# Kernel optimization log

Measured on AMD Instinct MI355X. Metric: run time of the kernel, lower is better.

Reference implementation:

```python
import jax, jax.numpy as jnp
import numpy as np

DIM = 1024
NUM_HEADS = 16
HEAD_DIM = DIM // NUM_HEADS


def _rope_tables(seq_len, dim, dtype):
    # matches llama_rotary_embedding: inv_freq over even indices of head_dim
    inv_freq = 1.0 / (10000.0 ** (jnp.arange(0, dim, 2, dtype=jnp.float32) / dim))
    t = jnp.arange(seq_len, dtype=jnp.float32)
    freqs = jnp.outer(t, inv_freq)  # [S, dim/2]
    return jnp.cos(freqs).astype(dtype), jnp.sin(freqs).astype(dtype)


def _apply_rope(x, cos_emb, sin_emb):
    # x: [B, H, S, hd]; takes interleaved halves, concatenates rotated halves
    x1 = x[..., 0::2]
    x2 = x[..., 1::2]
    return jnp.concatenate((x1 * cos_emb - x2 * sin_emb,
                            x1 * sin_emb + x2 * cos_emb), axis=-1)


def setup_inputs() -> dict:
    key = jax.random.key(0)
    k_x, k_qkv, k_out, k_b = jax.random.split(key, 4)
    B, S, D = 2, 2048, DIM
    x = jax.random.normal(k_x, (B, S, D), dtype=jnp.float32)
    # torch nn.Linear weights are [out_features, in_features]
    w_qkv = jax.random.normal(k_qkv, (3 * D, D), dtype=jnp.float32) * (1.0 / np.sqrt(D))
    w_out = jax.random.normal(k_out, (D, D), dtype=jnp.float32) * (1.0 / np.sqrt(D))
    b_out = jax.random.normal(k_b, (D,), dtype=jnp.float32) * 0.01
    return {"x": x, "w_qkv": w_qkv, "w_out": w_out, "b_out": b_out}


def reference(x, w_qkv, w_out, b_out):
    B, S, D = x.shape
    H, hd = NUM_HEADS, HEAD_DIM
    qkv = jnp.einsum('bsd,ed->bse', x, w_qkv)  # [B, S, 3D]
    q, k, v = jnp.split(qkv, 3, axis=-1)
    # [B, S, D] -> [B, H, S, hd]
    q, k, v = (t.reshape(B, S, H, hd).transpose(0, 2, 1, 3) for t in (q, k, v))
    cos_emb, sin_emb = _rope_tables(S, hd, x.dtype)  # [S, hd/2]
    q = _apply_rope(q, cos_emb, sin_emb)
    k = _apply_rope(k, cos_emb, sin_emb)
    scores = jnp.einsum('bhqd,bhkd->bhqk', q, k) / jnp.sqrt(jnp.asarray(hd, x.dtype))
    attn = jax.nn.softmax(scores, axis=-1)
    out = jnp.einsum('bhqk,bhkd->bhqd', attn, v)
    out = out.transpose(0, 2, 1, 3).reshape(B, S, D)
    return jnp.einsum('bsd,ed->bse', out, w_out) + b_out
```

## Files before the change

kernel.cpp:

```cpp
#include <hip/hip_runtime.h>
#include <math.h>

typedef __bf16 bf16_t;
typedef bf16_t bf16x8 __attribute__((ext_vector_type(8)));
typedef bf16_t bf16x4 __attribute__((ext_vector_type(4)));
typedef short  s16x4  __attribute__((ext_vector_type(4)));
typedef float  f32x4  __attribute__((ext_vector_type(4)));

#define DIM_   1024
#define NHEADS 16
#define HDIM   64
#define SEQ    2048
#define BATCH  2

#define QK_SCALE 0.18033688011112042f

__device__ __forceinline__ s16x4 as_s16x4(bf16x4 v) {
    union { bf16x4 b; s16x4 s; } u; u.b = v; return u.s;
}

__device__ __forceinline__ void gld16(const bf16_t* g, bf16_t* l) {
    __builtin_amdgcn_global_load_lds(
        (const __attribute__((address_space(1))) void*)g,
        (__attribute__((address_space(3))) void*)l, 16, 0, 0);
}

#define XCNT   (4096u * 1024u)
#define WQCNT  (3072u * 1024u)
#define WOCNT  (1024u * 1024u)
__global__ __launch_bounds__(256) void cast3(const float* __restrict__ s0,
                                             const float* __restrict__ s1,
                                             const float* __restrict__ s2,
                                             bf16_t* __restrict__ d0,
                                             bf16_t* __restrict__ d1,
                                             bf16_t* __restrict__ d2) {
    size_t i = ((size_t)blockIdx.x * 256 + threadIdx.x) * 8;
    const float* s; bf16_t* d; size_t off;
    if (i < XCNT)               { s = s0; d = d0; off = i; }
    else if (i < XCNT + WQCNT)  { s = s1; d = d1; off = i - XCNT; }
    else                        { s = s2; d = d2; off = i - XCNT - WQCNT; }
    float4 a = *(const float4*)(s + off);
    float4 b = *(const float4*)(s + off + 4);
    bf16x8 o = { (bf16_t)a.x, (bf16_t)a.y, (bf16_t)a.z, (bf16_t)a.w,
                 (bf16_t)b.x, (bf16_t)b.y, (bf16_t)b.z, (bf16_t)b.w };
    *(bf16x8*)(d + off) = o;
}

template <bool QKV>
__global__ __launch_bounds__(256) void gemm_lds(const bf16_t* __restrict__ A,
                                                const bf16_t* __restrict__ B,
                                                const float* __restrict__ bias,
                                                void* __restrict__ Cout,
                                                bf16_t* __restrict__ vt,
                                                int M, int N, int K) {
    __shared__ __align__(16) bf16_t As[2][128 * 32];
    __shared__ __align__(16) bf16_t Bs[2][128 * 32];
    const int tid  = threadIdx.x;
    const int m0   = blockIdx.y * 128;
    const int n0   = blockIdx.x * 128;
    const int w    = tid >> 6;
    const int lane = tid & 63;
    const int m16  = lane & 15;
    const int quad = lane >> 4;
    const int wm   = (w >> 1) * 64;
    const int wn   = (w & 1) * 64;
    const int lrow = lane >> 2;
    const int lcol = (lane & 3) * 8;

    const bf16_t* pa0 = A + (size_t)(m0 + w * 16 + lrow) * K + lcol;
    const bf16_t* pb0 = B + (size_t)(n0 + w * 16 + lrow) * K + lcol;
    const int sOffA0 = (w * 16) * 32;
    const int sOffA1 = (64 + w * 16) * 32;

    gld16(pa0, (bf16_t*)As + sOffA0);
    gld16(pa0 + (size_t)64 * K, (bf16_t*)As + sOffA1);
    gld16(pb0, (bf16_t*)Bs + sOffA0);
    gld16(pb0 + (size_t)64 * K, (bf16_t*)Bs + sOffA1);
    __syncthreads();

    f32x4 acc[4][4] = {};
    int buf = 0;

    for (int k0 = 0; k0 < K; k0 += 32) {
        const int nb = buf ^ 1;
        if (k0 + 32 < K) {
            gld16(pa0 + k0 + 32, (bf16_t*)As + nb * 4096 + sOffA0);
            gld16(pa0 + (size_t)64 * K + k0 + 32, (bf16_t*)As + nb * 4096 + sOffA1);
            gld16(pb0 + k0 + 32, (bf16_t*)Bs + nb * 4096 + sOffA0);
            gld16(pb0 + (size_t)64 * K + k0 + 32, (bf16_t*)Bs + nb * 4096 + sOffA1);
        }
        const bf16_t* sA = (const bf16_t*)As + buf * 4096;
        const bf16_t* sB = (const bf16_t*)Bs + buf * 4096;
        bf16x8 af[4], bfr[4];
#pragma unroll
        for (int i = 0; i < 4; ++i)
            af[i] = *(const bf16x8*)(sA + (wm + i * 16 + m16) * 32 + quad * 8);
#pragma unroll
        for (int j = 0; j < 4; ++j)
            bfr[j] = *(const bf16x8*)(sB + (wn + j * 16 + m16) * 32 + quad * 8);
#pragma unroll
        for (int i = 0; i < 4; ++i)
#pragma unroll
            for (int j = 0; j < 4; ++j)
                acc[i][j] = __builtin_amdgcn_mfma_f32_16x16x32_bf16(af[i], bfr[j], acc[i][j], 0, 0, 0);
        __syncthreads();
        buf = nb;
    }

    if (QKV && n0 >= 2 * DIM_) {
        const int b      = m0 >> 11;
        const int s_base = (m0 & (SEQ - 1)) + wm;
#pragma unroll
        for (int j = 0; j < 4; ++j) {
            const int cit = wn + j * 16 + m16;
            const int h   = ((n0 - 2 * DIM_) >> 6) + (cit >> 6);
            const int d   = cit & 63;
            bf16_t* vrow = vt + ((size_t)(b * 16 + h) * 64 + d) * SEQ + s_base;
#pragma unroll
            for (int i = 0; i < 4; ++i) {
                bf16x4 ov = { (bf16_t)acc[i][j][0], (bf16_t)acc[i][j][1],
                              (bf16_t)acc[i][j][2], (bf16_t)acc[i][j][3] };
                *(bf16x4*)(vrow + i * 16 + quad * 4) = ov;
            }
        }
    } else if (QKV) {
        bf16_t* C = (bf16_t*)Cout;
#pragma unroll
        for (int i = 0; i < 4; ++i)
#pragma unroll
            for (int j = 0; j < 4; ++j) {
                const int col = n0 + wn + j * 16 + m16;
#pragma unroll
                for (int r = 0; r < 4; ++r)
                    C[(size_t)(m0 + wm + i * 16 + quad * 4 + r) * N + col] = (bf16_t)acc[i][j][r];
            }
    } else {
        float* C = (float*)Cout;
#pragma unroll
        for (int j = 0; j < 4; ++j) {
            const int col = n0 + wn + j * 16 + m16;
            const float bv = bias[col];
#pragma unroll
            for (int i = 0; i < 4; ++i)
#pragma unroll
                for (int r = 0; r < 4; ++r)
                    C[(size_t)(m0 + wm + i * 16 + quad * 4 + r) * N + col] = acc[i][j][r] + bv;
        }
    }
}

__global__ __launch_bounds__(256) void gemm_out64(const bf16_t* __restrict__ A,
                                                  const bf16_t* __restrict__ B,
                                                  const float* __restrict__ bias,
                                                  float* __restrict__ C,
                                                  int M, int N, int K) {
    __shared__ __align__(16) bf16_t As[2][128 * 32];
    __shared__ __align__(16) bf16_t Bs[2][64 * 32];
    const int tid  = threadIdx.x;
    const int m0   = blockIdx.y * 128;
    const int n0   = blockIdx.x * 64;
    const int w    = tid >> 6;
    const int lane = tid & 63;
    const int m16  = lane & 15;
    const int quad = lane >> 4;
    const int wm   = (w >> 1) * 64;
    const int wn   = (w & 1) * 32;
    const int lrow = lane >> 2;
    const int lcol = (lane & 3) * 8;

    const bf16_t* pa0 = A + (size_t)(m0 + w * 16 + lrow) * K + lcol;
    const bf16_t* pb0 = B + (size_t)(n0 + w * 16 + lrow) * K + lcol;
    const int sOff0 = (w * 16) * 32;
    const int sOff1 = (64 + w * 16) * 32;

    gld16(pa0, (bf16_t*)As + sOff0);
    gld16(pa0 + (size_t)64 * K, (bf16_t*)As + sOff1);
    gld16(pb0, (bf16_t*)Bs + sOff0);
    __syncthreads();

    f32x4 acc[4][2] = {};
    int buf = 0;

    for (int k0 = 0; k0 < K; k0 += 32) {
        const int nb = buf ^ 1;
        if (k0 + 32 < K) {
            gld16(pa0 + k0 + 32, (bf16_t*)As + nb * 4096 + sOff0);
            gld16(pa0 + (size_t)64 * K + k0 + 32, (bf16_t*)As + nb * 4096 + sOff1);
            gld16(pb0 + k0 + 32, (bf16_t*)Bs + nb * 2048 + sOff0);
        }
        const bf16_t* sA = (const bf16_t*)As + buf * 4096;
        const bf16_t* sB = (const bf16_t*)Bs + buf * 2048;
        bf16x8 af[4], bfr[2];
#pragma unroll
        for (int i = 0; i < 4; ++i)
            af[i] = *(const bf16x8*)(sA + (wm + i * 16 + m16) * 32 + quad * 8);
#pragma unroll
        for (int j = 0; j < 2; ++j)
            bfr[j] = *(const bf16x8*)(sB + (wn + j * 16 + m16) * 32 + quad * 8);
#pragma unroll
        for (int i = 0; i < 4; ++i)
#pragma unroll
            for (int j = 0; j < 2; ++j)
                acc[i][j] = __builtin_amdgcn_mfma_f32_16x16x32_bf16(af[i], bfr[j], acc[i][j], 0, 0, 0);
        __syncthreads();
        buf = nb;
    }

#pragma unroll
    for (int j = 0; j < 2; ++j) {
        const int col = n0 + wn + j * 16 + m16;
        const float bv = bias[col];
#pragma unroll
        for (int i = 0; i < 4; ++i)
#pragma unroll
            for (int r = 0; r < 4; ++r)
                C[(size_t)(m0 + wm + i * 16 + quad * 4 + r) * N + col] = acc[i][j][r] + bv;
    }
}

__global__ __launch_bounds__(256) void rope_bf16(bf16_t* __restrict__ qkv) {
    __shared__ float ctab[8][32];
    __shared__ float stab[8][32];
    const int tid = threadIdx.x;
    const int sl  = tid >> 5, j = tid & 31;
    const int s   = (int)((blockIdx.x * 8 + sl) & (SEQ - 1));
    const float freq = exp2f(-0.41524101186092029f * (float)j);
    float sn, cs;
    sincosf((float)s * freq, &sn, &cs);
    ctab[sl][j] = cs;
    stab[sl][j] = sn;
    __syncthreads();

    const int gid   = blockIdx.x * 256 + tid;
    const int m     = gid >> 5;
    const int rr    = gid & 31;
    const int which = rr >> 4;
    const int hh    = rr & 15;
    const float osc = (which == 0) ? QK_SCALE : 1.0f;

    bf16_t* p = qkv + (size_t)m * (3 * DIM_) + which * DIM_ + hh * HDIM;
    union { bf16_t e[64]; bf16x8 v[8]; } X, O;
#pragma unroll
    for (int i = 0; i < 8; ++i) X.v[i] = *(const bf16x8*)(p + i * 8);
#pragma unroll
    for (int t = 0; t < 32; ++t) {
        const float x1 = (float)X.e[2 * t];
        const float x2 = (float)X.e[2 * t + 1];
        const float c  = ctab[sl][t];
        const float s2 = stab[sl][t];
        O.e[t]      = (bf16_t)((x1 * c - x2 * s2) * osc);
        O.e[32 + t] = (bf16_t)((x1 * s2 + x2 * c) * osc);
    }
#pragma unroll
    for (int i = 0; i < 8; ++i) *(bf16x8*)(p + i * 8) = O.v[i];
}

__global__ __launch_bounds__(256) void attn_mfma(const bf16_t* __restrict__ qkv,
                                                 const bf16_t* __restrict__ vt,
                                                 bf16_t* __restrict__ out) {
    __shared__ __align__(16) char smem[37888];
    bf16_t* Ks0  = (bf16_t*)smem;
    bf16_t* Vt0  = (bf16_t*)(smem + 9216);
    bf16_t* Ks1  = (bf16_t*)(smem + 18432);
    bf16_t* Vt1  = (bf16_t*)(smem + 27648);
    float*  Ored = (float*)smem;
    float*  Lred = (float*)(smem + 36864);

    const int tid  = threadIdx.x;
    const int w    = tid >> 6;
    const int lane = tid & 63;
    const int m16  = lane & 15;
    const int quad = lane >> 4;
    const int bh   = blockIdx.y;
    const int b    = bh >> 4;
    const int hh   = bh & 15;
    const int q0   = blockIdx.x * 64;

    const size_t rs = 3 * DIM_;
    const bf16_t* qbase = qkv + (size_t)(b * SEQ) * rs + hh * HDIM;
    const bf16_t* kbase = qbase + DIM_;
    const bf16_t* vtg   = vt + (size_t)bh * 64 * SEQ;

    bf16x8 qf[4][2];
#pragma unroll
    for (int n = 0; n < 4; ++n)
#pragma unroll
        for (int kt = 0; kt < 2; ++kt)
            qf[n][kt] = *(const bf16x8*)(qbase + (size_t)(q0 + n * 16 + m16) * rs + kt * 32 + quad * 8);

    f32x4 o[4][4] = {};
    float lp[4] = {};

    const int srow = tid >> 3;
    const int sc8  = (tid & 7) * 8;

    bf16x8 kreg[2], vreg[2];

#pragma unroll
    for (int p = 0; p < 2; ++p) {
        const int row = srow + p * 32;
        kreg[p] = *(const bf16x8*)(kbase + (size_t)row * rs + sc8);
        vreg[p] = *(const bf16x8*)(vtg + (size_t)row * SEQ + sc8);
    }
#pragma unroll
    for (int p = 0; p < 2; ++p) {
        const int row = srow + p * 32;
        *(bf16x8*)(&Ks0[row * 72 + sc8]) = kreg[p];
        *(bf16x8*)(&Vt0[row * 72 + sc8]) = vreg[p];
    }
    __syncthreads();

    const bf16_t* kg0 = kbase + (size_t)(64 + srow) * rs + sc8;
    const bf16_t* kg1 = kg0 + (size_t)32 * rs;
    const bf16_t* vg0 = vtg + (size_t)srow * SEQ + 64 + sc8;
    const bf16_t* vg1 = vg0 + (size_t)32 * SEQ;
    const size_t kadv = (size_t)64 * rs;

#define ATTN_BODY(T, KS, VS, KSN, VSN)                                             \
    do {                                                                           \
        const int tt = (T);                                                        \
        if (tt < 31) {                                                             \
            kreg[0] = *(const bf16x8*)(kg0);                                       \
            kreg[1] = *(const bf16x8*)(kg1);                                       \
            vreg[0] = *(const bf16x8*)(vg0);                                       \
            vreg[1] = *(const bf16x8*)(vg1);                                       \
            kg0 += kadv; kg1 += kadv; vg0 += 64; vg1 += 64;                        \
        }                                                                          \
        bf16x8 ak0 = *(const bf16x8*)(&KS[(w * 16 + m16) * 72 + 0 * 32 + quad * 8]); \
        bf16x8 ak1 = *(const bf16x8*)(&KS[(w * 16 + m16) * 72 + 1 * 32 + quad * 8]); \
        bf16x4 va[4];                                                              \
        _Pragma("unroll")                                                          \
        for (int ds = 0; ds < 4; ++ds)                                             \
            va[ds] = *(const bf16x4*)(&VS[(ds * 16 + m16) * 72 + w * 16 + quad * 4]); \
        s16x4 pb[4];                                                               \
        _Pragma("unroll")                                                          \
        for (int n = 0; n < 4; ++n) {                                              \
            f32x4 c = {};                                                          \
            c = __builtin_amdgcn_mfma_f32_16x16x32_bf16(ak0, qf[n][0], c, 0, 0, 0); \
            c = __builtin_amdgcn_mfma_f32_16x16x32_bf16(ak1, qf[n][1], c, 0, 0, 0); \
            bf16x4 pv;                                                             \
            _Pragma("unroll")                                                      \
            for (int r = 0; r < 4; ++r) {                                          \
                const float pp = __builtin_amdgcn_exp2f(c[r]);                     \
                lp[n] += pp;                                                       \
                pv[r] = (bf16_t)pp;                                                \
            }                                                                      \
            pb[n] = as_s16x4(pv);                                                  \
        }                                                                          \
        __builtin_amdgcn_s_setprio(1);                                             \
        _Pragma("unroll")                                                          \
        for (int ds = 0; ds < 4; ++ds)                                             \
            _Pragma("unroll")                                                      \
            for (int n = 0; n < 4; ++n)                                            \
                o[ds][n] = __builtin_amdgcn_mfma_f32_16x16x16bf16_1k(               \
                    as_s16x4(va[ds]), pb[n], o[ds][n], 0, 0, 0);                   \
        __builtin_amdgcn_s_setprio(0);                                             \
        if (tt < 31) {                                                             \
            _Pragma("unroll")                                                      \
            for (int p = 0; p < 2; ++p) {                                          \
                const int row = srow + p * 32;                                     \
                *(bf16x8*)(&KSN[row * 72 + sc8]) = kreg[p];                        \
                *(bf16x8*)(&VSN[row * 72 + sc8]) = vreg[p];                        \
            }                                                                      \
        }                                                                          \
        __syncthreads();                                                           \
    } while (0)

    for (int t = 0; t < 32; t += 2) {
        ATTN_BODY(t,     Ks0, Vt0, Ks1, Vt1);
        ATTN_BODY(t + 1, Ks1, Vt1, Ks0, Vt0);
    }
#undef ATTN_BODY

#pragma unroll
    for (int n = 0; n < 4; ++n) {
        lp[n] += __shfl_xor(lp[n], 16);
        lp[n] += __shfl_xor(lp[n], 32);
    }
    if (quad == 0) {
#pragma unroll
        for (int n = 0; n < 4; ++n) Lred[w * 64 + n * 16 + m16] = lp[n];
    }
    __syncthreads();
    const float linv = 1.0f / (Lred[lane] + Lred[64 + lane] + Lred[128 + lane] + Lred[192 + lane]);

    const size_t obase = (size_t)(b * SEQ + q0 + lane) * DIM_ + hh * HDIM;
#pragma unroll
    for (int p = 0; p < 4; ++p) {
        __syncthreads();
#pragma unroll
        for (int n = 0; n < 4; ++n)
#pragma unroll
            for (int r = 0; r < 4; ++r)
                Ored[w * 1040 + (quad * 4 + r) * 65 + n * 16 + m16] = o[p][n][r];
        __syncthreads();
        union { bf16_t e[4]; bf16x4 v; } ob;
#pragma unroll
        for (int d = 0; d < 4; ++d) {
            const int dd = w * 4 + d;
            const float v = Ored[dd * 65 + lane] + Ored[1040 + dd * 65 + lane] +
                            Ored[2080 + dd * 65 + lane] + Ored[3120 + dd * 65 + lane];
            ob.e[d] = (bf16_t)(v * linv);
        }
        *(bf16x4*)(out + obase + p * 16 + w * 4) = ob.v;
    }
}

extern "C" void kernel_launch(void* const* d_in, const int* in_sizes, int n_in,
                              void* d_out, int out_size, void* d_ws, size_t ws_size,
                              hipStream_t stream) {
    const float* x     = (const float*)d_in[0];
    const float* w_qkv = (const float*)d_in[1];
    const float* w_out = (const float*)d_in[2];
    const float* b_out = (const float*)d_in[3];
    float* out = (float*)d_out;

    const int M = BATCH * SEQ;

    bf16_t* qkv_b  = (bf16_t*)d_ws;
    bf16_t* attn_b = qkv_b + (size_t)M * 3 * DIM_;
    bf16_t* vt_b   = attn_b + (size_t)M * DIM_;
    bf16_t* xb     = vt_b + (size_t)BATCH * NHEADS * HDIM * SEQ;
    bf16_t* wqkvb  = xb + (size_t)M * DIM_;
    bf16_t* woutb  = wqkvb + (size_t)3 * DIM_ * DIM_;

    cast3<<<(XCNT + WQCNT + WOCNT) / (256 * 8), 256, 0, stream>>>(
        x, w_qkv, w_out, xb, wqkvb, woutb);

    gemm_lds<true><<<dim3(3 * DIM_ / 128, M / 128), 256, 0, stream>>>(
        xb, wqkvb, nullptr, qkv_b, vt_b, M, 3 * DIM_, DIM_);

    rope_bf16<<<(M * 2 * NHEADS) / 256, 256, 0, stream>>>(qkv_b);

    attn_mfma<<<dim3(SEQ / 64, BATCH * NHEADS), 256, 0, stream>>>(qkv_b, vt_b, attn_b);

    gemm_out64<<<dim3(DIM_ / 64, M / 128), 256, 0, stream>>>(
        attn_b, woutb, b_out, out, M, DIM_, DIM_);
}
```

Baseline: 206.8 us.

## Software-pipeline attention loop: overlap PV MFMAs of previous tile with QK of current

Restructures the attention inner loop so each iteration computes QK scores and exp for the current K/V tile while issuing the PV MFMAs for the previous tile's probabilities and V fragments. A prologue handles tile 0 and an epilogue drains the last PV. The aim is to break the dependency between exp conversion and the PV MFMAs so the matrix units stay busy. In exchange it keeps two sets of P and V fragments in registers, which raises register pressure and could lower occupancy.

```diff
diff --git a/kernel.cpp b/kernel.cpp
--- a/kernel.cpp
+++ b/kernel.cpp
@@ -316,7 +316,45 @@
     const bf16_t* vg1 = vg0 + (size_t)32 * SEQ;
     const size_t kadv = (size_t)64 * rs;
 
-#define ATTN_BODY(T, KS, VS, KSN, VSN)                                             \
+    s16x4  pbA[4], pbB[4];
+    bf16x4 vaA[4], vaB[4];
+
+    {
+        kreg[0] = *(const bf16x8*)(kg0);
+        kreg[1] = *(const bf16x8*)(kg1);
+        vreg[0] = *(const bf16x8*)(vg0);
+        vreg[1] = *(const bf16x8*)(vg1);
+        kg0 += kadv; kg1 += kadv; vg0 += 64; vg1 += 64;
+
+        bf16x8 ak0 = *(const bf16x8*)(&Ks0[(w * 16 + m16) * 72 + 0 * 32 + quad * 8]);
+        bf16x8 ak1 = *(const bf16x8*)(&Ks0[(w * 16 + m16) * 72 + 1 * 32 + quad * 8]);
+#pragma unroll
+        for (int ds = 0; ds < 4; ++ds)
+            vaA[ds] = *(const bf16x4*)(&Vt0[(ds * 16 + m16) * 72 + w * 16 + quad * 4]);
+#pragma unroll
+        for (int n = 0; n < 4; ++n) {
+            f32x4 c = {};
+            c = __builtin_amdgcn_mfma_f32_16x16x32_bf16(ak0, qf[n][0], c, 0, 0, 0);
+            c = __builtin_amdgcn_mfma_f32_16x16x32_bf16(ak1, qf[n][1], c, 0, 0, 0);
+            bf16x4 pv;
+#pragma unroll
+            for (int r = 0; r < 4; ++r) {
+                const float pp = __builtin_amdgcn_exp2f(c[r]);
+                lp[n] += pp;
+                pv[r] = (bf16_t)pp;
+            }
+            pbA[n] = as_s16x4(pv);
+        }
+#pragma unroll
+        for (int p = 0; p < 2; ++p) {
+            const int row = srow + p * 32;
+            *(bf16x8*)(&Ks1[row * 72 + sc8]) = kreg[p];
+            *(bf16x8*)(&Vt1[row * 72 + sc8]) = vreg[p];
+        }
+        __syncthreads();
+    }
+
+#define ATTN_BODY(T, KS, VS, KSN, VSN, PBc, VAc, PBp, VAp)                         \
     do {                                                                           \
         const int tt = (T);                                                        \
         if (tt < 31) {                                                             \
@@ -328,11 +366,9 @@
         }                                                                          \
         bf16x8 ak0 = *(const bf16x8*)(&KS[(w * 16 + m16) * 72 + 0 * 32 + quad * 8]); \
         bf16x8 ak1 = *(const bf16x8*)(&KS[(w * 16 + m16) * 72 + 1 * 32 + quad * 8]); \
-        bf16x4 va[4];                                                              \
         _Pragma("unroll")                                                          \
         for (int ds = 0; ds < 4; ++ds)                                             \
-            va[ds] = *(const bf16x4*)(&VS[(ds * 16 + m16) * 72 + w * 16 + quad * 4]); \
-        s16x4 pb[4];                                                               \
+            VAc[ds] = *(const bf16x4*)(&VS[(ds * 16 + m16) * 72 + w * 16 + quad * 4]); \
         _Pragma("unroll")                                                          \
         for (int n = 0; n < 4; ++n) {                                              \
             f32x4 c = {};                                                          \
@@ -345,7 +381,7 @@
                 lp[n] += pp;                                                       \
                 pv[r] = (bf16_t)pp;                                                \
             }                                                                      \
-            pb[n] = as_s16x4(pv);                                                  \
+            PBc[n] = as_s16x4(pv);                                                 \
         }                                                                          \
         __builtin_amdgcn_s_setprio(1);                                             \
         _Pragma("unroll")                                                          \
@@ -353,7 +389,7 @@
             _Pragma("unroll")                                                      \
             for (int n = 0; n < 4; ++n)                                            \
                 o[ds][n] = __builtin_amdgcn_mfma_f32_16x16x16bf16_1k(               \
-                    as_s16x4(va[ds]), pb[n], o[ds][n], 0, 0, 0);                   \
+                    as_s16x4(VAp[ds]), PBp[n], o[ds][n], 0, 0, 0);                 \
         __builtin_amdgcn_s_setprio(0);                                             \
         if (tt < 31) {                                                             \
             _Pragma("unroll")                                                      \
@@ -366,11 +402,21 @@
         __syncthreads();                                                           \
     } while (0)
 
-    for (int t = 0; t < 32; t += 2) {
-        ATTN_BODY(t,     Ks0, Vt0, Ks1, Vt1);
-        ATTN_BODY(t + 1, Ks1, Vt1, Ks0, Vt0);
-    }
+    for (int t = 1; t < 31; t += 2) {
+        ATTN_BODY(t,     Ks1, Vt1, Ks0, Vt0, pbB, vaB, pbA, vaA);
+        ATTN_BODY(t + 1, Ks0, Vt0, Ks1, Vt1, pbA, vaA, pbB, vaB);
+    }
+    ATTN_BODY(31, Ks1, Vt1, Ks0, Vt0, pbB, vaB, pbA, vaA);
 #undef ATTN_BODY
+
+    __builtin_amdgcn_s_setprio(1);
+#pragma unroll
+    for (int ds = 0; ds < 4; ++ds)
+#pragma unroll
+        for (int n = 0; n < 4; ++n)
+            o[ds][n] = __builtin_amdgcn_mfma_f32_16x16x16bf16_1k(
+                as_s16x4(vaB[ds]), pbB[n], o[ds][n], 0, 0, 0);
+    __builtin_amdgcn_s_setprio(0);
 
 #pragma unroll
     for (int n = 0; n < 4; ++n) {
```

Measured after the change: 204.5 us. Within noise of the previous version (-1.1%).

## Store K per-head contiguous and V in MFMA tile order, drop attention LDS staging

Applied to the files above, without the earlier changes.

The QKV GEMM epilogue now writes Q, K (head-major, contiguous per sequence row) and V (pre-tiled into 16-key blocks matching the MFMA operand layout) into separate buffers. The attention kernel then loads K and V fragments straight from global memory into registers with a two-tile register double-buffer, removing the LDS staging and per-tile __syncthreads. This cuts shared memory use and barriers and may raise occupancy, but every wave now reads K/V from global/L2 independently instead of sharing an LDS copy. The K epilogue also uses scattered scalar stores.

```diff
diff --git a/kernel.cpp b/kernel.cpp
--- a/kernel.cpp
+++ b/kernel.cpp
@@ -46,11 +46,10 @@
     *(bf16x8*)(d + off) = o;
 }
 
-template <bool QKV>
-__global__ __launch_bounds__(256) void gemm_lds(const bf16_t* __restrict__ A,
+__global__ __launch_bounds__(256) void gemm_qkv(const bf16_t* __restrict__ A,
                                                 const bf16_t* __restrict__ B,
-                                                const float* __restrict__ bias,
-                                                void* __restrict__ Cout,
+                                                bf16_t* __restrict__ qb,
+                                                bf16_t* __restrict__ kt,
                                                 bf16_t* __restrict__ vt,
                                                 int M, int N, int K) {
     __shared__ __align__(16) bf16_t As[2][128 * 32];
@@ -107,44 +106,46 @@
         buf = nb;
     }
 
-    if (QKV && n0 >= 2 * DIM_) {
-        const int b      = m0 >> 11;
-        const int s_base = (m0 & (SEQ - 1)) + wm;
+    const int b = m0 >> 11;
+    if (n0 < DIM_) {
+#pragma unroll
+        for (int i = 0; i < 4; ++i)
+#pragma unroll
+            for (int j = 0; j < 4; ++j) {
+                const int col = n0 + wn + j * 16 + m16;
+#pragma unroll
+                for (int r = 0; r < 4; ++r)
+                    qb[(size_t)(m0 + wm + i * 16 + quad * 4 + r) * DIM_ + col] = (bf16_t)acc[i][j][r];
+            }
+    } else if (n0 < 2 * DIM_) {
 #pragma unroll
         for (int j = 0; j < 4; ++j) {
-            const int cit = wn + j * 16 + m16;
-            const int h   = ((n0 - 2 * DIM_) >> 6) + (cit >> 6);
-            const int d   = cit & 63;
-            bf16_t* vrow = vt + ((size_t)(b * 16 + h) * 64 + d) * SEQ + s_base;
+            const int n = n0 - DIM_ + wn + j * 16 + m16;
+            const int h = n >> 6;
+            const int d = n & 63;
+            bf16_t* kb = kt + (size_t)(b * 16 + h) * SEQ * 64 + d;
 #pragma unroll
             for (int i = 0; i < 4; ++i) {
+                const int s = (m0 & (SEQ - 1)) + wm + i * 16 + quad * 4;
+#pragma unroll
+                for (int r = 0; r < 4; ++r)
+                    kb[(size_t)(s + r) * 64] = (bf16_t)acc[i][j][r];
+            }
+        }
+    } else {
+#pragma unroll
+        for (int j = 0; j < 4; ++j) {
+            const int n = n0 - 2 * DIM_ + wn + j * 16 + m16;
+            const int h = n >> 6;
+            const int d = n & 63;
+#pragma unroll
+            for (int i = 0; i < 4; ++i) {
+                const int s0 = (m0 & (SEQ - 1)) + wm + i * 16;
+                const int kb = s0 >> 4;
                 bf16x4 ov = { (bf16_t)acc[i][j][0], (bf16_t)acc[i][j][1],
                               (bf16_t)acc[i][j][2], (bf16_t)acc[i][j][3] };
-                *(bf16x4*)(vrow + i * 16 + quad * 4) = ov;
+                *(bf16x4*)(vt + ((size_t)((b * 16 + h) * 128 + kb) * 64 + d) * 16 + quad * 4) = ov;
             }
-        }
-    } else if (QKV) {
-        bf16_t* C = (bf16_t*)Cout;
-#pragma unroll
-        for (int i = 0; i < 4; ++i)
-#pragma unroll
-            for (int j = 0; j < 4; ++j) {
-                const int col = n0 + wn + j * 16 + m16;
-#pragma unroll
-                for (int r = 0; r < 4; ++r)
-                    C[(size_t)(m0 + wm + i * 16 + quad * 4 + r) * N + col] = (bf16_t)acc[i][j][r];
-            }
-    } else {
-        float* C = (float*)Cout;
-#pragma unroll
-        for (int j = 0; j < 4; ++j) {
-            const int col = n0 + wn + j * 16 + m16;
-            const float bv = bias[col];
-#pragma unroll
-            for (int i = 0; i < 4; ++i)
-#pragma unroll
-                for (int r = 0; r < 4; ++r)
-                    C[(size_t)(m0 + wm + i * 16 + quad * 4 + r) * N + col] = acc[i][j][r] + bv;
         }
     }
 }
@@ -218,7 +219,8 @@
     }
 }
 
-__global__ __launch_bounds__(256) void rope_bf16(bf16_t* __restrict__ qkv) {
+__global__ __launch_bounds__(256) void rope_bf16(bf16_t* __restrict__ qb,
+                                                 bf16_t* __restrict__ kt) {
     __shared__ float ctab[8][32];
     __shared__ float stab[8][32];
     const int tid = threadIdx.x;
@@ -236,9 +238,17 @@
     const int rr    = gid & 31;
     const int which = rr >> 4;
     const int hh    = rr & 15;
-    const float osc = (which == 0) ? QK_SCALE : 1.0f;
-
-    bf16_t* p = qkv + (size_t)m * (3 * DIM_) + which * DIM_ + hh * HDIM;
+
+    bf16_t* p;
+    float osc;
+    if (which == 0) {
+        p = qb + (size_t)m * DIM_ + hh * HDIM;
+        osc = QK_SCALE;
+    } else {
+        const int b = m >> 11;
+        p = kt + ((size_t)(b * 16 + hh) * SEQ + (m & (SEQ - 1))) * 64;
+        osc = 1.0f;
+    }
     union { bf16_t e[64]; bf16x8 v[8]; } X, O;
 #pragma unroll
     for (int i = 0; i < 8; ++i) X.v[i] = *(const bf16x8*)(p + i * 8);
@@ -255,16 +265,13 @@
     for (int i = 0; i < 8; ++i) *(bf16x8*)(p + i * 8) = O.v[i];
 }
 
-__global__ __launch_bounds__(256) void attn_mfma(const bf16_t* __restrict__ qkv,
+__global__ __launch_bounds__(256) void attn_mfma(const bf16_t* __restrict__ qb,
+                                                 const bf16_t* __restrict__ kt,
                                                  const bf16_t* __restrict__ vt,
                                                  bf16_t* __restrict__ out) {
-    __shared__ __align__(16) char smem[37888];
-    bf16_t* Ks0  = (bf16_t*)smem;
-    bf16_t* Vt0  = (bf16_t*)(smem + 9216);
-    bf16_t* Ks1  = (bf16_t*)(smem + 18432);
-    bf16_t* Vt1  = (bf16_t*)(smem + 27648);
-    float*  Ored = (float*)smem;
-    float*  Lred = (float*)(smem + 36864);
+    __shared__ __align__(16) char smem[17664];
+    float* Ored = (float*)smem;
+    float* Lred = (float*)(smem + 16640);
 
     const int tid  = threadIdx.x;
     const int w    = tid >> 6;
@@ -276,68 +283,39 @@
     const int hh   = bh & 15;
     const int q0   = blockIdx.x * 64;
 
-    const size_t rs = 3 * DIM_;
-    const bf16_t* qbase = qkv + (size_t)(b * SEQ) * rs + hh * HDIM;
-    const bf16_t* kbase = qbase + DIM_;
-    const bf16_t* vtg   = vt + (size_t)bh * 64 * SEQ;
-
     bf16x8 qf[4][2];
 #pragma unroll
     for (int n = 0; n < 4; ++n)
 #pragma unroll
-        for (int kt = 0; kt < 2; ++kt)
-            qf[n][kt] = *(const bf16x8*)(qbase + (size_t)(q0 + n * 16 + m16) * rs + kt * 32 + quad * 8);
+        for (int c = 0; c < 2; ++c)
+            qf[n][c] = *(const bf16x8*)(qb + (size_t)(b * SEQ + q0 + n * 16 + m16) * DIM_ +
+                                        hh * HDIM + c * 32 + quad * 8);
 
     f32x4 o[4][4] = {};
     float lp[4] = {};
 
-    const int srow = tid >> 3;
-    const int sc8  = (tid & 7) * 8;
-
-    bf16x8 kreg[2], vreg[2];
-
-#pragma unroll
-    for (int p = 0; p < 2; ++p) {
-        const int row = srow + p * 32;
-        kreg[p] = *(const bf16x8*)(kbase + (size_t)row * rs + sc8);
-        vreg[p] = *(const bf16x8*)(vtg + (size_t)row * SEQ + sc8);
-    }
-#pragma unroll
-    for (int p = 0; p < 2; ++p) {
-        const int row = srow + p * 32;
-        *(bf16x8*)(&Ks0[row * 72 + sc8]) = kreg[p];
-        *(bf16x8*)(&Vt0[row * 72 + sc8]) = vreg[p];
-    }
-    __syncthreads();
-
-    const bf16_t* kg0 = kbase + (size_t)(64 + srow) * rs + sc8;
-    const bf16_t* kg1 = kg0 + (size_t)32 * rs;
-    const bf16_t* vg0 = vtg + (size_t)srow * SEQ + 64 + sc8;
-    const bf16_t* vg1 = vg0 + (size_t)32 * SEQ;
-    const size_t kadv = (size_t)64 * rs;
-
-#define ATTN_BODY(T, KS, VS, KSN, VSN)                                             \
+    const bf16_t* kp = kt + ((size_t)bh * SEQ + w * 16 + m16) * 64 + quad * 8;
+    const bf16_t* vp = vt + (((size_t)bh * 128 + w) * 64 + m16) * 16 + quad * 4;
+
+#define LOAD_TILE(AK0, AK1, VA)                                \
+    do {                                                       \
+        AK0 = *(const bf16x8*)(kp);                            \
+        AK1 = *(const bf16x8*)(kp + 32);                       \
+        VA[0] = *(const bf16x4*)(vp);                          \
+        VA[1] = *(const bf16x4*)(vp + 256);                    \
+        VA[2] = *(const bf16x4*)(vp + 512);                    \
+        VA[3] = *(const bf16x4*)(vp + 768);                    \
+        kp += 4096; vp += 4096;                                \
+    } while (0)
+
+#define COMPUTE_TILE(AK0, AK1, VA)                                                 \
     do {                                                                           \
-        const int tt = (T);                                                        \
-        if (tt < 31) {                                                             \
-            kreg[0] = *(const bf16x8*)(kg0);                                       \
-            kreg[1] = *(const bf16x8*)(kg1);                                       \
-            vreg[0] = *(const bf16x8*)(vg0);                                       \
-            vreg[1] = *(const bf16x8*)(vg1);                                       \
-            kg0 += kadv; kg1 += kadv; vg0 += 64; vg1 += 64;                        \
-        }                                                                          \
-        bf16x8 ak0 = *(const bf16x8*)(&KS[(w * 16 + m16) * 72 + 0 * 32 + quad * 8]); \
-        bf16x8 ak1 = *(const bf16x8*)(&KS[(w * 16 + m16) * 72 + 1 * 32 + quad * 8]); \
-        bf16x4 va[4];                                                              \
-        _Pragma("unroll")                                                          \
-        for (int ds = 0; ds < 4; ++ds)                                             \
-            va[ds] = *(const bf16x4*)(&VS[(ds * 16 + m16) * 72 + w * 16 + quad * 4]); \
         s16x4 pb[4];                                                               \
         _Pragma("unroll")                                                          \
         for (int n = 0; n < 4; ++n) {                                              \
             f32x4 c = {};                                                          \
-            c = __builtin_amdgcn_mfma_f32_16x16x32_bf16(ak0, qf[n][0], c, 0, 0, 0); \
-            c = __builtin_amdgcn_mfma_f32_16x16x32_bf16(ak1, qf[n][1], c, 0, 0, 0); \
+            c = __builtin_amdgcn_mfma_f32_16x16x32_bf16(AK0, qf[n][0], c, 0, 0, 0); \
+            c = __builtin_amdgcn_mfma_f32_16x16x32_bf16(AK1, qf[n][1], c, 0, 0, 0); \
             bf16x4 pv;                                                             \
             _Pragma("unroll")                                                      \
             for (int r = 0; r < 4; ++r) {                                          \
@@ -353,24 +331,23 @@
             _Pragma("unroll")                                                      \
             for (int n = 0; n < 4; ++n)                                            \
                 o[ds][n] = __builtin_amdgcn_mfma_f32_16x16x16bf16_1k(               \
-                    as_s16x4(va[ds]), pb[n], o[ds][n], 0, 0, 0);                   \
+                    as_s16x4(VA[ds]), pb[n], o[ds][n], 0, 0, 0);                   \
         __builtin_amdgcn_s_setprio(0);                                             \
-        if (tt < 31) {                                                             \
-            _Pragma("unroll")                                                      \
-            for (int p = 0; p < 2; ++p) {                                          \
-                const int row = srow + p * 32;                                     \
-                *(bf16x8*)(&KSN[row * 72 + sc8]) = kreg[p];                        \
-                *(bf16x8*)(&VSN[row * 72 + sc8]) = vreg[p];                        \
-            }                                                                      \
-        }                                                                          \
-        __syncthreads();                                                           \
     } while (0)
 
+    bf16x8 akA0, akA1, akB0, akB1;
+    bf16x4 vaA[4], vaB[4];
+
+    LOAD_TILE(akA0, akA1, vaA);
     for (int t = 0; t < 32; t += 2) {
-        ATTN_BODY(t,     Ks0, Vt0, Ks1, Vt1);
-        ATTN_BODY(t + 1, Ks1, Vt1, Ks0, Vt0);
-    }
-#undef ATTN_BODY
+        LOAD_TILE(akB0, akB1, vaB);
+        COMPUTE_TILE(akA0, akA1, vaA);
+        if (t + 2 < 32)
+            LOAD_TILE(akA0, akA1, vaA);
+        COMPUTE_TILE(akB0, akB1, vaB);
+    }
+#undef LOAD_TILE
+#undef COMPUTE_TILE
 
 #pragma unroll
     for (int n = 0; n < 4; ++n) {
@@ -417,22 +394,23 @@
 
     const int M = BATCH * SEQ;
 
-    bf16_t* qkv_b  = (bf16_t*)d_ws;
-    bf16_t* attn_b = qkv_b + (size_t)M * 3 * DIM_;
-    bf16_t* vt_b   = attn_b + (size_t)M * DIM_;
-    bf16_t* xb     = vt_b + (size_t)BATCH * NHEADS * HDIM * SEQ;
+    bf16_t* q_b    = (bf16_t*)d_ws;
+    bf16_t* attn_b = q_b + (size_t)M * DIM_;
+    bf16_t* kt_b   = attn_b + (size_t)M * DIM_;
+    bf16_t* vt_b   = kt_b + (size_t)M * DIM_;
+    bf16_t* xb     = vt_b + (size_t)M * DIM_;
     bf16_t* wqkvb  = xb + (size_t)M * DIM_;
     bf16_t* woutb  = wqkvb + (size_t)3 * DIM_ * DIM_;
 
     cast3<<<(XCNT + WQCNT + WOCNT) / (256 * 8), 256, 0, stream>>>(
         x, w_qkv, w_out, xb, wqkvb, woutb);
 
-    gemm_lds<true><<<dim3(3 * DIM_ / 128, M / 128), 256, 0, stream>>>(
-        xb, wqkvb, nullptr, qkv_b, vt_b, M, 3 * DIM_, DIM_);
-
-    rope_bf16<<<(M * 2 * NHEADS) / 256, 256, 0, stream>>>(qkv_b);
-
-    attn_mfma<<<dim3(SEQ / 64, BATCH * NHEADS), 256, 0, stream>>>(qkv_b, vt_b, attn_b);
+    gemm_qkv<<<dim3(3 * DIM_ / 128, M / 128), 256, 0, stream>>>(
+        xb, wqkvb, q_b, kt_b, vt_b, M, 3 * DIM_, DIM_);
+
+    rope_bf16<<<(M * 2 * NHEADS) / 256, 256, 0, stream>>>(q_b, kt_b);
+
+    attn_mfma<<<dim3(SEQ / 64, BATCH * NHEADS), 256, 0, stream>>>(q_b, kt_b, vt_b, attn_b);
 
     gemm_out64<<<dim3(DIM_ / 64, M / 128), 256, 0, stream>>>(
         attn_b, woutb, b_out, out, M, DIM_, DIM_);
```

Result: no change. 209.4 us (+1.2%).
